# Kernel optimization log

Hardware: AMD Instinct MI355X
Metric: run time of the kernel (lower is better)

The kernel has to match this reference:

```python
import jax, jax.numpy as jnp
import numpy as np

N0 = N1 = 50000
E = 800000
IN = 128
OUT = 128
H = 8
DK = OUT // H  # 16
SQRT_DK = float(np.sqrt(DK))
T = 2  # node types


def setup_inputs() -> dict:
    key = jax.random.key(0)
    ks = jax.random.split(key, 24)
    s = 1.0 / np.sqrt(IN)
    inp = {
        "feat0": jax.random.normal(ks[0], (N0, IN), jnp.float32),
        "feat1": jax.random.normal(ks[1], (N1, IN), jnp.float32),
        "ev0": jax.random.uniform(ks[2], (E,), jnp.float32),
        "ev1": jax.random.uniform(ks[3], (E,), jnp.float32),
        "ev2": jax.random.uniform(ks[4], (E,), jnp.float32),
        "src0": jax.random.randint(ks[5], (E,), 0, N0),   # t0 -> t1
        "dst0": jax.random.randint(ks[6], (E,), 0, N1),
        "src1": jax.random.randint(ks[7], (E,), 0, N1),   # t1 -> t0
        "dst1": jax.random.randint(ks[8], (E,), 0, N0),
        "src2": jax.random.randint(ks[9], (E,), 0, N0),   # t0 -> t0
        "dst2": jax.random.randint(ks[10], (E,), 0, N0),
        # per-node-type parameters, stacked over T types
        "Kw": jax.random.normal(ks[11], (T, IN, OUT), jnp.float32) * s,
        "Kb": jnp.zeros((T, OUT), jnp.float32),
        "Qw": jax.random.normal(ks[12], (T, IN, OUT), jnp.float32) * s,
        "Qb": jnp.zeros((T, OUT), jnp.float32),
        "Vw": jax.random.normal(ks[13], (T, IN, OUT), jnp.float32) * s,
        "Vb": jnp.zeros((T, OUT), jnp.float32),
        "Aw": jax.random.normal(ks[14], (T, OUT, OUT), jnp.float32) * s,
        "Ab": jnp.zeros((T, OUT), jnp.float32),
        "ew": jax.random.normal(ks[15], (), jnp.float32),  # e_linear weight (1x1)
        "eb": jnp.zeros((), jnp.float32),                  # e_linear bias
        "skip": jnp.ones((T,), jnp.float32),
    }
    return inp


def _etype_agg(feat_s, feat_d, ts, td, src, dst, ev, n_dst,
               Kw, Kb, Qw, Qb, Vw, Vb, ew, eb):
    """One canonical etype: gather q.k per edge, edge_softmax over dst, u_mul_e + sum."""
    k = (feat_s @ Kw[ts] + Kb[ts]).reshape(-1, H, DK)
    v = (feat_s @ Vw[ts] + Vb[ts]).reshape(-1, H, DK)
    q = (feat_d @ Qw[td] + Qb[td]).reshape(-1, H, DK)
    # per-edge dot(q[dst], k[src]) over d_k -> [E, H]
    score = jnp.einsum('ehd,ehd->eh', q[dst], k[src])
    ea = ev[:, None] * ew + eb                     # e_linear on scalar edge feature, [E,1]
    score = score * ea / SQRT_DK                   # [E, H]
    # segmented softmax over incoming edges per destination node, per head
    m = jax.ops.segment_max(score, dst, num_segments=n_dst)
    ex = jnp.exp(score - m[dst])
    z = jax.ops.segment_sum(ex, dst, num_segments=n_dst)
    attn = ex / z[dst]                             # [E, H]
    msg = v[src] * attn[:, :, None]                # [E, H, DK]
    return jax.ops.segment_sum(msg, dst, num_segments=n_dst)  # [n_dst, H, DK]


def reference(feat0, feat1, ev0, ev1, ev2, src0, dst0, src1, dst1, src2, dst2,
              Kw, Kb, Qw, Qb, Vw, Vb, Aw, Ab, ew, eb, skip):
    # etype (t0,e0,t1)
    agg1 = _etype_agg(feat0, feat1, 0, 1, src0, dst0, ev0, N1,
                      Kw, Kb, Qw, Qb, Vw, Vb, ew, eb)
    # etypes targeting t0: (t1,e1,t0) and (t0,e2,t0); cross_reducer='mean'
    agg0a = _etype_agg(feat1, feat0, 1, 0, src1, dst1, ev1, N0,
                       Kw, Kb, Qw, Qb, Vw, Vb, ew, eb)
    agg0b = _etype_agg(feat0, feat0, 0, 0, src2, dst2, ev2, N0,
                       Kw, Kb, Qw, Qb, Vw, Vb, ew, eb)
    agg0 = 0.5 * (agg0a + agg0b)

    def _out(agg, feat, nid):
        t = agg.reshape(-1, OUT)
        trans = t @ Aw[nid] + Ab[nid]              # dropout omitted (eval mode)
        alpha = jax.nn.sigmoid(skip[nid])
        return trans * alpha + feat * (1.0 - alpha)

    h0 = _out(agg0, feat0, 0)
    h1 = _out(agg1, feat1, 1)
    return (h0, h1)
```

## Files before the change

### kernel.cpp

```cpp
#include <hip/hip_runtime.h>
#include <hip/hip_bf16.h>
#include <hip/hip_fp16.h>
#include <math.h>


#define NDIM 128
#define NRNG 32
#define NBK 512
#define UNITS (NBK * 4)
#define HSPAN 2048

typedef __attribute__((ext_vector_type(8))) short short8;
typedef __attribute__((ext_vector_type(4))) float f32x4;
typedef __attribute__((ext_vector_type(2))) _Float16 half2v;

__device__ __forceinline__ float bf2f(unsigned short u) {
    union { unsigned int i; float f; } x; x.i = ((unsigned int)u) << 16; return x.f;
}
__device__ __forceinline__ unsigned short f2bf(float f) {
    unsigned int u = __float_as_uint(f);
    unsigned int r = (u + 0x7FFFu + ((u >> 16) & 1u)) >> 16;
    return (unsigned short)r;
}
__device__ __forceinline__ int range_of(int d, int n) {
    return (int)(((long long)d * NRNG) / n);
}
union U4h { ushort4 u; struct { half2v a, b; } h; };

__global__ __launch_bounds__(256) void wt_prep(const float* __restrict__ Kw, const float* __restrict__ Qw,
                                               const float* __restrict__ Vw, const float* __restrict__ Aw,
                                               unsigned short* __restrict__ Wtbuf)
{
    const int b = blockIdx.x;
    const int t = b >> 2, m = b & 3;
    const float* src = (m == 0 ? Kw : m == 1 ? Qw : m == 2 ? Vw : Aw) + (size_t)t * 16384;
    unsigned short* dst = Wtbuf + (size_t)b * 16384;
    const int tid = threadIdx.x;
    __shared__ float tile[64][132];
#pragma unroll
    for (int h = 0; h < 2; ++h) {
        const int k0 = h * 64;
        for (int idx = tid; idx < 64 * 32; idx += 256) {
            const int kr = idx >> 5;
            const int c4 = (idx & 31) * 4;
            const float4 v = *(const float4*)(src + (size_t)(k0 + kr) * 128 + c4);
            tile[kr][c4 + 0] = v.x; tile[kr][c4 + 1] = v.y;
            tile[kr][c4 + 2] = v.z; tile[kr][c4 + 3] = v.w;
        }
        __syncthreads();
        for (int idx = tid; idx < 128 * 16; idx += 256) {
            const int nn = idx >> 4;
            const int kk4 = (idx & 15) * 4;
            ushort4 o;
            o.x = f2bf(tile[kk4 + 0][nn]); o.y = f2bf(tile[kk4 + 1][nn]);
            o.z = f2bf(tile[kk4 + 2][nn]); o.w = f2bf(tile[kk4 + 3][nn]);
            *(ushort4*)(dst + (size_t)nn * 128 + k0 + kk4) = o;
        }
        __syncthreads();
    }
}

__global__ __launch_bounds__(256) void gemm_kqv(
    const float* __restrict__ feat0, const float* __restrict__ feat1,
    const unsigned short* __restrict__ Wtbuf,
    const float* __restrict__ Kb, const float* __restrict__ Qb, const float* __restrict__ Vb,
    unsigned short* __restrict__ K0o, unsigned short* __restrict__ Q0o, unsigned short* __restrict__ V0o,
    unsigned short* __restrict__ K1o, unsigned short* __restrict__ Q1o, unsigned short* __restrict__ V1o,
    int n0, int n1, int blocks0)
{
    const int b = blockIdx.x;
    const bool t1 = (b >= blocks0);
    const float* feat = t1 ? feat1 : feat0;
    const int n = t1 ? n1 : n0;
    const int boff = t1 ? NDIM : 0;
    const unsigned short* Wt = Wtbuf + (t1 ? 4 * 16384 : 0);
    unsigned short* outs[3];
    outs[0] = t1 ? K1o : K0o; outs[1] = t1 ? Q1o : Q0o; outs[2] = t1 ? V1o : V0o;
    const float* biases[3] = {Kb + boff, Qb + boff, Vb + boff};

    const int tid = threadIdx.x;
    const int w = tid >> 6, lane = tid & 63;
    const int r16 = lane & 15, kg = lane >> 4;
    const int brow = (t1 ? b - blocks0 : b) * 64;
    const int arow = min(brow + w * 16 + r16, n - 1);

    __shared__ float sacc[64][129];

    short8 afr[4];
#pragma unroll
    for (int k0i = 0; k0i < 4; ++k0i) {
        const float* ap = feat + (size_t)arow * NDIM + k0i * 32 + kg * 8;
        const float4 lo = *(const float4*)ap;
        const float4 hi = *(const float4*)(ap + 4);
        short8 a;
        a[0] = (short)f2bf(lo.x); a[1] = (short)f2bf(lo.y);
        a[2] = (short)f2bf(lo.z); a[3] = (short)f2bf(lo.w);
        a[4] = (short)f2bf(hi.x); a[5] = (short)f2bf(hi.y);
        a[6] = (short)f2bf(hi.z); a[7] = (short)f2bf(hi.w);
        afr[k0i] = a;
    }
    const int c8 = (lane & 15) * 8;
#pragma unroll
    for (int m = 0; m < 3; ++m) {
        const unsigned short* wt = Wt + (size_t)m * 16384;
        f32x4 acc[8];
#pragma unroll
        for (int c = 0; c < 8; ++c) acc[c] = (f32x4){0.f, 0.f, 0.f, 0.f};
#pragma unroll
        for (int k0i = 0; k0i < 4; ++k0i)
#pragma unroll
            for (int c = 0; c < 8; ++c) {
                const short8 bb = *(const short8*)(wt + (size_t)(16 * c + r16) * NDIM + k0i * 32 + kg * 8);
                acc[c] = __builtin_amdgcn_mfma_f32_16x16x32_bf16(afr[k0i], bb, acc[c], 0, 0, 0);
            }
        __syncthreads();
#pragma unroll
        for (int c = 0; c < 8; ++c)
#pragma unroll
            for (int j = 0; j < 4; ++j)
                sacc[w * 16 + kg * 4 + j][16 * c + r16] = acc[c][j];
        __syncthreads();
        const float4 blo = *(const float4*)(biases[m] + c8);
        const float4 bhi = *(const float4*)(biases[m] + c8 + 4);
        const float bias8[8] = {blo.x, blo.y, blo.z, blo.w, bhi.x, bhi.y, bhi.z, bhi.w};
#pragma unroll
        for (int j = 0; j < 4; ++j) {
            const int rloc = w * 16 + (lane >> 4) + j * 4;
            const int grow = brow + rloc;
            if (grow < n) {
                short8 o;
#pragma unroll
                for (int i = 0; i < 8; ++i) {
                    const float x = sacc[rloc][c8 + i] + bias8[i];
                    o[i] = (m < 2) ? (short)__half_as_ushort(__float2half(x))
                                   : (short)f2bf(x);
                }
                *(short8*)(outs[m] + (size_t)grow * NDIM + c8) = o;
            }
        }
    }
}

__global__ __launch_bounds__(256) void gemm_out(
    const unsigned short* __restrict__ aggb0a, const unsigned short* __restrict__ aggb0b,
    const unsigned short* __restrict__ aggb1,
    const unsigned short* __restrict__ Wtbuf, const float* __restrict__ Ab,
    const float* __restrict__ feat0, const float* __restrict__ feat1,
    const float* __restrict__ skip, float* __restrict__ out,
    int n0, int n1, int blocks0)
{
    const int b = blockIdx.x;
    const bool t1 = (b >= blocks0);
    const int n = t1 ? n1 : n0;
    const unsigned short* A1 = t1 ? aggb1 : aggb0a;
    const unsigned short* A2 = t1 ? (const unsigned short*)nullptr : aggb0b;
    const unsigned short* Wt = Wtbuf + (t1 ? 7 : 3) * 16384;
    const float* bias = Ab + (t1 ? NDIM : 0);
    const float* feat = t1 ? feat1 : feat0;
    float* C = out + (t1 ? (size_t)n0 * NDIM : 0);
    const int nid = t1 ? 1 : 0;

    const int tid = threadIdx.x;
    const int w = tid >> 6, lane = tid & 63;
    const int r16 = lane & 15, kg = lane >> 4;
    const int brow = (t1 ? b - blocks0 : b) * 64;
    const int arow = min(brow + w * 16 + r16, n - 1);

    __shared__ float sacc[64][129];

    short8 afr[4];
#pragma unroll
    for (int k0i = 0; k0i < 4; ++k0i) {
        short8 a = *(const short8*)(A1 + (size_t)arow * NDIM + k0i * 32 + kg * 8);
        if (!t1) {
            const short8 bb = *(const short8*)(A2 + (size_t)arow * NDIM + k0i * 32 + kg * 8);
#pragma unroll
            for (int j = 0; j < 8; ++j) {
                const float v = 0.5f * (bf2f((unsigned short)a[j]) + bf2f((unsigned short)bb[j]));
                a[j] = (short)f2bf(v);
            }
        }
        afr[k0i] = a;
    }
    f32x4 acc[8];
#pragma unroll
    for (int c = 0; c < 8; ++c) acc[c] = (f32x4){0.f, 0.f, 0.f, 0.f};
#pragma unroll
    for (int k0i = 0; k0i < 4; ++k0i)
#pragma unroll
        for (int c = 0; c < 8; ++c) {
            const short8 bb = *(const short8*)(Wt + (size_t)(16 * c + r16) * NDIM + k0i * 32 + kg * 8);
            acc[c] = __builtin_amdgcn_mfma_f32_16x16x32_bf16(afr[k0i], bb, acc[c], 0, 0, 0);
        }
    __syncthreads();
#pragma unroll
    for (int c = 0; c < 8; ++c)
#pragma unroll
        for (int j = 0; j < 4; ++j)
            sacc[w * 16 + kg * 4 + j][16 * c + r16] = acc[c][j];
    __syncthreads();

    const float sk = skip[nid];
    const float alpha = 1.f / (1.f + __expf(-sk));
    const float beta = 1.f - alpha;
    const int c8 = (lane & 15) * 8;
    const float4 blo = *(const float4*)(bias + c8);
    const float4 bhi = *(const float4*)(bias + c8 + 4);
#pragma unroll
    for (int j = 0; j < 4; ++j) {
        const int rloc = w * 16 + (lane >> 4) + j * 4;
        const int grow = brow + rloc;
        if (grow < n) {
            const float4 fa = *(const float4*)(feat + (size_t)grow * NDIM + c8);
            const float4 fb = *(const float4*)(feat + (size_t)grow * NDIM + c8 + 4);
            float4 oa, ob;
            oa.x = (sacc[rloc][c8 + 0] + blo.x) * alpha + fa.x * beta;
            oa.y = (sacc[rloc][c8 + 1] + blo.y) * alpha + fa.y * beta;
            oa.z = (sacc[rloc][c8 + 2] + blo.z) * alpha + fa.z * beta;
            oa.w = (sacc[rloc][c8 + 3] + blo.w) * alpha + fa.w * beta;
            ob.x = (sacc[rloc][c8 + 4] + bhi.x) * alpha + fb.x * beta;
            ob.y = (sacc[rloc][c8 + 5] + bhi.y) * alpha + fb.y * beta;
            ob.z = (sacc[rloc][c8 + 6] + bhi.z) * alpha + fb.z * beta;
            ob.w = (sacc[rloc][c8 + 7] + bhi.w) * alpha + fb.w * beta;
            *(float4*)(C + (size_t)grow * NDIM + c8) = oa;
            *(float4*)(C + (size_t)grow * NDIM + c8 + 4) = ob;
        }
    }
}

__global__ __launch_bounds__(256) void bucket_count(
    const int* __restrict__ d0, int E0, const int* __restrict__ d1, int E1,
    const int* __restrict__ d2, int E2, int n0, int n1, int* __restrict__ cnts)
{
    const int seg = blockIdx.y;
    const int* dst = seg == 0 ? d0 : (seg == 1 ? d1 : d2);
    const int E = seg == 0 ? E0 : (seg == 1 ? E1 : E2);
    const int ns = seg == 0 ? n1 : n0;
    const int unit = blockIdx.x * 4 + (threadIdx.x >> 6);
    const int lane = threadIdx.x & 63;
    const int span = (E + UNITS - 1) / UNITS;
    const int b = unit * span;
    const int e = min(b + span, E);

    int run[NRNG];
#pragma unroll
    for (int r0 = 0; r0 < NRNG; ++r0) run[r0] = 0;
    for (int i0 = b; i0 < e; i0 += 64) {
        const int i = i0 + lane;
        const bool v = i < e;
        const int d = v ? dst[i] : 0;
        const unsigned int r = v ? (unsigned int)range_of(d, ns) : 0xFFu;
#pragma unroll
        for (int r0 = 0; r0 < NRNG; ++r0)
            run[r0] += __popcll(__ballot(r == (unsigned int)r0));
    }
    if (lane == 0) {
        int* c = cnts + ((size_t)seg * UNITS + unit) * NRNG;
#pragma unroll
        for (int r0 = 0; r0 < NRNG; ++r0) c[r0] = run[r0];
    }
}

__global__ __launch_bounds__(256) void bucket_scan(int* __restrict__ cnts, int* __restrict__ rcur)
{
    const int seg = blockIdx.x >> 5;
    const int r = blockIdx.x & 31;
    const int t = threadIdx.x, lane = t & 63, w = t >> 6;

    int v[8];
    int run = 0;
#pragma unroll
    for (int j = 0; j < 8; ++j) {
        const int u = t * 8 + j;
        const int x = cnts[((size_t)seg * UNITS + u) * NRNG + r];
        v[j] = run;
        run += x;
    }
    const int tsum = run;
    int x = tsum;
#pragma unroll
    for (int o = 1; o < 64; o <<= 1) {
        const int y = __shfl_up(x, o);
        if (lane >= o) x += y;
    }
    const int wexc = x - tsum;
    __shared__ int wsum[4];
    if (lane == 63) wsum[w] = x;
    __syncthreads();
    int wbase = 0;
    for (int i = 0; i < w; ++i) wbase += wsum[i];
    const int base = wbase + wexc;
#pragma unroll
    for (int j = 0; j < 8; ++j) {
        const int u = t * 8 + j;
        cnts[((size_t)seg * UNITS + u) * NRNG + r] = base + v[j];
    }
    if (t == 255) rcur[seg * NRNG + r] = base + tsum;
}

__global__ __launch_bounds__(256) void bucket_write(
    const int* __restrict__ d0, const int* __restrict__ s0, const float* __restrict__ e0, int E0,
    const int* __restrict__ d1, const int* __restrict__ s1, const float* __restrict__ e1, int E1,
    const int* __restrict__ d2, const int* __restrict__ s2, const float* __restrict__ e2, int E2,
    int n0, int n1, const float* __restrict__ ew, const float* __restrict__ eb,
    const int* __restrict__ cnts, uint2* __restrict__ stg, int cap)
{
    const int seg = blockIdx.y;
    const int* dst = seg == 0 ? d0 : (seg == 1 ? d1 : d2);
    const int* src = seg == 0 ? s0 : (seg == 1 ? s1 : s2);
    const float* ev = seg == 0 ? e0 : (seg == 1 ? e1 : e2);
    const int E = seg == 0 ? E0 : (seg == 1 ? E1 : E2);
    const int ns = seg == 0 ? n1 : n0;
    const int unit = blockIdx.x * 4 + (threadIdx.x >> 6);
    const int lane = threadIdx.x & 63;
    const int span = (E + UNITS - 1) / UNITS;
    const int b = unit * span;
    const int e = min(b + span, E);
    const float LOG2E = 1.4426950408889634f;
    const float ews = ew[0] * 0.25f * LOG2E;
    const float ebs = eb[0] * 0.25f * LOG2E;
    uint2* sbase = stg + (size_t)seg * NRNG * cap;

    int run[NRNG];
    {
        const int* c = cnts + ((size_t)seg * UNITS + unit) * NRNG;
#pragma unroll
        for (int r0 = 0; r0 < NRNG; ++r0) run[r0] = c[r0];
    }
    for (int i0 = b; i0 < e; i0 += 64) {
        const int i = i0 + lane;
        const bool v = i < e;
        int d = 0, s = 0; float ee = 0.f;
        if (v) { d = dst[i]; s = src[i]; ee = ev[i]; }
        const unsigned int r = v ? (unsigned int)range_of(d, ns) : 0xFFu;
#pragma unroll
        for (int r0 = 0; r0 < NRNG; ++r0) {
            const unsigned long long m = __ballot(r == (unsigned int)r0);
            if (m == 0ull) continue;
            if (r == (unsigned int)r0) {
                const int off = run[r0] + __popcll(m & ((1ull << lane) - 1ull));
                sbase[(size_t)r0 * cap + off] =
                    make_uint2((unsigned int)d | ((unsigned int)s << 16), __float_as_uint(ee * ews + ebs));
            }
            run[r0] += __popcll(m);
        }
    }
}

__global__ __launch_bounds__(1024) void sortB(
    const uint2* __restrict__ stg, int cap, const int* __restrict__ rcur,
    int nA, int* __restrict__ offA, unsigned int* __restrict__ gA,
    int nB, int* __restrict__ offB, unsigned int* __restrict__ gB,
    int nC, int* __restrict__ offC, unsigned int* __restrict__ gC)
{
    const int seg = blockIdx.y;
    const int r = blockIdx.x;
    const int n = seg == 0 ? nA : (seg == 1 ? nB : nC);
    int* off = seg == 0 ? offA : (seg == 1 ? offB : offC);
    unsigned int* edg = seg == 0 ? gA : (seg == 1 ? gB : gC);
    const int cnt = rcur[seg * NRNG + r];
    const uint2* s = stg + ((size_t)seg * NRNG + r) * cap;
    const int dbase = (int)(((long long)r * n + NRNG - 1) / NRNG);
    const int dnext = (int)(((long long)(r + 1) * n + NRNG - 1) / NRNG);
    const int span = dnext - dbase;
    int ebase = 0;
    for (int i = 0; i < r; ++i) ebase += rcur[seg * NRNG + i];

    __shared__ int hist[HSPAN];
    __shared__ int wsum[16];
    const int tid = threadIdx.x, lane = tid & 63, wid = tid >> 6;

    for (int i = tid; i < span; i += 1024) hist[i] = 0;
    __syncthreads();
    for (int i = tid; i < cnt; i += 1024)
        atomicAdd(&hist[(int)(s[i].x & 0xFFFFu) - dbase], 1);
    __syncthreads();
    const int C = (span + 1023) >> 10;
    int v[4];
    int run = 0;
    const int b0 = tid * C;
#pragma unroll 4
    for (int j = 0; j < C; ++j) {
        const int i = b0 + j;
        const int x = (i < span) ? hist[i] : 0;
        v[j] = run;
        run += x;
    }
    int x = run;
#pragma unroll
    for (int o = 1; o < 64; o <<= 1) {
        const int y = __shfl_up(x, o);
        if (lane >= o) x += y;
    }
    if (lane == 63) wsum[wid] = x;
    __syncthreads();
    int wbase = 0;
    for (int i = 0; i < wid; ++i) wbase += wsum[i];
    const int tb = ebase + wbase + (x - run);
#pragma unroll 4
    for (int j = 0; j < C; ++j) {
        const int i = b0 + j;
        if (i < span) hist[i] = tb + v[j];
    }
    __syncthreads();
    for (int i = tid; i < span; i += 1024) off[dbase + i] = hist[i];
    if (r == NRNG - 1 && tid == 0) off[n] = ebase + cnt;
    __syncthreads();
    for (int i = tid; i < cnt; i += 1024) {
        const uint2 e = s[i];
        const int d = (int)(e.x & 0xFFFFu);
        const int p = atomicAdd(&hist[d - dbase], 1);
        const float wf = __uint_as_float(e.y);
        const __half hh = __float2half(wf);
        edg[p] = (e.x >> 16) | ((unsigned int)__half_as_ushort(hh) << 16);
    }
}

__global__ __launch_bounds__(256) void edge_agg3(
    const int* __restrict__ off0, const unsigned int* __restrict__ edg0,
    const unsigned short* __restrict__ K0e, const unsigned short* __restrict__ Q0e,
    const unsigned short* __restrict__ V0e, unsigned short* __restrict__ out0, int nd0,
    const int* __restrict__ off1, const unsigned int* __restrict__ edg1,
    const unsigned short* __restrict__ K1e, const unsigned short* __restrict__ Q1e,
    const unsigned short* __restrict__ V1e, unsigned short* __restrict__ out1, int nd1,
    const int* __restrict__ off2, const unsigned int* __restrict__ edg2,
    const unsigned short* __restrict__ K2e, const unsigned short* __restrict__ Q2e,
    const unsigned short* __restrict__ V2e, unsigned short* __restrict__ out2, int nd2)
{
    const int seg = blockIdx.y;
    const int* off = seg == 0 ? off0 : (seg == 1 ? off1 : off2);
    const unsigned int* edg = seg == 0 ? edg0 : (seg == 1 ? edg1 : edg2);
    const unsigned short* K = seg == 0 ? K0e : (seg == 1 ? K1e : K2e);
    const unsigned short* Q = seg == 0 ? Q0e : (seg == 1 ? Q1e : Q2e);
    const unsigned short* V = seg == 0 ? V0e : (seg == 1 ? V1e : V2e);
    unsigned short* aggb = seg == 0 ? out0 : (seg == 1 ? out1 : out2);
    const int n_dst = seg == 0 ? nd0 : (seg == 1 ? nd1 : nd2);

    const int wv = (blockIdx.x * blockDim.x + threadIdx.x) >> 6;
    const int lane = threadIdx.x & 63;
    const int half = lane >> 5, l5 = lane & 31;
    const int dst = 2 * wv + half;
    const bool valid = dst < n_dst;
    int beg = 0, len = 0;
    if (valid) { beg = off[dst]; len = off[dst + 1] - beg; }
    const int maxLen = max(len, __shfl_xor(len, 32));
    if (maxLen == 0) {
        if (valid) *(ushort4*)(aggb + (size_t)dst * NDIM + 4 * l5) = (ushort4){0, 0, 0, 0};
        return;
    }
    U4h q;
    q.u = make_ushort4(0, 0, 0, 0);
    if (valid) q.u = *(const ushort4*)(Q + (size_t)dst * NDIM + 4 * l5);
    const half2v q01 = q.h.a, q23 = q.h.b;

    float zA = 0.f, aA0 = 0.f, aA1 = 0.f, aA2 = 0.f, aA3 = 0.f;
    float zB = 0.f, aB0 = 0.f, aB1 = 0.f, aB2 = 0.f, aB3 = 0.f;

    unsigned int ec = (l5 < len) ? edg[beg + l5] : 0u;
    for (int t0 = 0; t0 < maxLen; t0 += 32) {
        unsigned int en = 0u;
        const int t0n = t0 + 32;
        if (t0n < maxLen && t0n + l5 < len) en = edg[beg + t0n + l5];
        const int lim = min(32, maxLen - t0);
        for (int u = 0; u < lim; u += 2) {
            const int sl0 = (half << 5) + u;
            const unsigned int v0 = (unsigned int)__shfl((int)ec, sl0);
            const unsigned int v1 = (unsigned int)__shfl((int)ec, sl0 + 1);
            const bool act0 = (t0 + u) < len;
            const bool act1 = (u + 1 < lim) && ((t0 + u + 1) < len);
            const int s0 = (int)(v0 & 0xFFFFu);
            const int s1 = (int)(v1 & 0xFFFFu);
            const float w0 = __half2float(__ushort_as_half((unsigned short)(v0 >> 16)));
            const float w1 = __half2float(__ushort_as_half((unsigned short)(v1 >> 16)));
            U4h k0u, k1u;
            k0u.u = *(const ushort4*)(K + (size_t)s0 * NDIM + 4 * l5);
            k1u.u = *(const ushort4*)(K + (size_t)s1 * NDIM + 4 * l5);
            const ushort4 vr0 = *(const ushort4*)(V + (size_t)s0 * NDIM + 4 * l5);
            const ushort4 vr1 = *(const ushort4*)(V + (size_t)s1 * NDIM + 4 * l5);
#if __has_builtin(__builtin_amdgcn_fdot2)
            float d0 = __builtin_amdgcn_fdot2(k0u.h.a, q01, 0.f, false);
            d0 = __builtin_amdgcn_fdot2(k0u.h.b, q23, d0, false);
            float d1 = __builtin_amdgcn_fdot2(k1u.h.a, q01, 0.f, false);
            d1 = __builtin_amdgcn_fdot2(k1u.h.b, q23, d1, false);
#else
            float d0 = (float)k0u.h.a[0] * (float)q01[0] + (float)k0u.h.a[1] * (float)q01[1]
                     + (float)k0u.h.b[0] * (float)q23[0] + (float)k0u.h.b[1] * (float)q23[1];
            float d1 = (float)k1u.h.a[0] * (float)q01[0] + (float)k1u.h.a[1] * (float)q01[1]
                     + (float)k1u.h.b[0] * (float)q23[0] + (float)k1u.h.b[1] * (float)q23[1];
#endif
            d0 += __shfl_xor(d0, 1);
            d1 += __shfl_xor(d1, 1);
            d0 += __shfl_xor(d0, 2);
            d1 += __shfl_xor(d1, 2);
            const float p0 = act0 ? exp2f(d0 * w0) : 0.f;
            const float p1 = act1 ? exp2f(d1 * w1) : 0.f;
            zA += p0;
            aA0 += p0 * bf2f(vr0.x); aA1 += p0 * bf2f(vr0.y);
            aA2 += p0 * bf2f(vr0.z); aA3 += p0 * bf2f(vr0.w);
            zB += p1;
            aB0 += p1 * bf2f(vr1.x); aB1 += p1 * bf2f(vr1.y);
            aB2 += p1 * bf2f(vr1.z); aB3 += p1 * bf2f(vr1.w);
        }
        ec = en;
    }
    if (valid) {
        const float z = zA + zB;
        const float inv = (len > 0) ? 1.f / z : 0.f;
        ushort4 o;
        o.x = f2bf((aA0 + aB0) * inv); o.y = f2bf((aA1 + aB1) * inv);
        o.z = f2bf((aA2 + aB2) * inv); o.w = f2bf((aA3 + aB3) * inv);
        *(ushort4*)(aggb + (size_t)dst * NDIM + 4 * l5) = o;
    }
}

extern "C" void kernel_launch(void* const* d_in, const int* in_sizes, int n_in,
                              void* d_out, int out_size, void* d_ws, size_t ws_size,
                              hipStream_t stream)
{
    const float* feat0 = (const float*)d_in[0];
    const float* feat1 = (const float*)d_in[1];
    const float* ev0 = (const float*)d_in[2];
    const float* ev1 = (const float*)d_in[3];
    const float* ev2 = (const float*)d_in[4];
    const int* src0 = (const int*)d_in[5];
    const int* dst0 = (const int*)d_in[6];
    const int* src1 = (const int*)d_in[7];
    const int* dst1 = (const int*)d_in[8];
    const int* src2 = (const int*)d_in[9];
    const int* dst2 = (const int*)d_in[10];
    const float* Kw = (const float*)d_in[11];
    const float* Kb = (const float*)d_in[12];
    const float* Qw = (const float*)d_in[13];
    const float* Qb = (const float*)d_in[14];
    const float* Vw = (const float*)d_in[15];
    const float* Vb = (const float*)d_in[16];
    const float* Aw = (const float*)d_in[17];
    const float* Ab = (const float*)d_in[18];
    const float* ew = (const float*)d_in[19];
    const float* eb = (const float*)d_in[20];
    const float* skip = (const float*)d_in[21];

    const int n0 = in_sizes[0] / NDIM;
    const int n1 = in_sizes[1] / NDIM;
    const int E0 = in_sizes[5];
    const int E1 = in_sizes[7];
    const int E2 = in_sizes[9];
    if (max(n0, n1) > 65504) return;
    const int Emax = max(E0, max(E1, E2));
    const int cap = Emax / NRNG + 8192;

    auto rup = [](size_t b) { return (b + 255) & ~size_t(255); };
    const size_t need =
        rup((size_t)8 * 16384 * 2) +
        rup((size_t)n0 * NDIM * 2) * 3 +
        rup((size_t)n1 * NDIM * 2) * 3 +
        rup((size_t)n1 * NDIM * 2) +
        rup((size_t)n0 * NDIM * 2) * 2 +
        rup((size_t)(n1 + 1) * 4) +
        rup((size_t)(n0 + 1) * 4) * 2 +
        rup((size_t)128 * 4) +
        rup((size_t)3 * UNITS * NRNG * 4) +
        rup((size_t)3 * NRNG * cap * 8) +
        rup((size_t)E0 * 4) + rup((size_t)E1 * 4) + rup((size_t)E2 * 4);
    if (ws_size < need) return;

    char* p = (char*)d_ws;
    auto alloc = [&](size_t bytes) -> char* {
        char* r = p;
        p += (bytes + 255) & ~size_t(255);
        return r;
    };
    unsigned short* Wtbuf = (unsigned short*)alloc((size_t)8 * 16384 * 2);
    unsigned short* K0 = (unsigned short*)alloc((size_t)n0 * NDIM * 2);
    unsigned short* Q0 = (unsigned short*)alloc((size_t)n0 * NDIM * 2);
    unsigned short* V0 = (unsigned short*)alloc((size_t)n0 * NDIM * 2);
    unsigned short* K1 = (unsigned short*)alloc((size_t)n1 * NDIM * 2);
    unsigned short* Q1 = (unsigned short*)alloc((size_t)n1 * NDIM * 2);
    unsigned short* V1 = (unsigned short*)alloc((size_t)n1 * NDIM * 2);
    unsigned short* aggb1  = (unsigned short*)alloc((size_t)n1 * NDIM * 2);
    unsigned short* aggb0a = (unsigned short*)alloc((size_t)n0 * NDIM * 2);
    unsigned short* aggb0b = (unsigned short*)alloc((size_t)n0 * NDIM * 2);
    int* off0 = (int*)alloc((size_t)(n1 + 1) * 4);
    int* off1 = (int*)alloc((size_t)(n0 + 1) * 4);
    int* off2 = (int*)alloc((size_t)(n0 + 1) * 4);
    int* rcur = (int*)alloc((size_t)128 * 4);
    int* cnts = (int*)alloc((size_t)3 * UNITS * NRNG * 4);
    uint2* stg = (uint2*)alloc((size_t)3 * NRNG * cap * 8);
    unsigned int* edg0 = (unsigned int*)alloc((size_t)E0 * 4);
    unsigned int* edg1 = (unsigned int*)alloc((size_t)E1 * 4);
    unsigned int* edg2 = (unsigned int*)alloc((size_t)E2 * 4);

    dim3 blk(256);
    const int blocks0 = (n0 + 63) / 64, blocks1 = (n1 + 63) / 64;

    wt_prep<<<8, 256, 0, stream>>>(Kw, Qw, Vw, Aw, Wtbuf);
    gemm_kqv<<<blocks0 + blocks1, blk, 0, stream>>>(feat0, feat1, Wtbuf, Kb, Qb, Vb,
                                                    K0, Q0, V0, K1, Q1, V1, n0, n1, blocks0);

    bucket_count<<<dim3(NBK, 3), blk, 0, stream>>>(dst0, E0, dst1, E1, dst2, E2, n0, n1, cnts);
    bucket_scan<<<3 * NRNG, blk, 0, stream>>>(cnts, rcur);
    bucket_write<<<dim3(NBK, 3), blk, 0, stream>>>(dst0, src0, ev0, E0,
                                                   dst1, src1, ev1, E1,
                                                   dst2, src2, ev2, E2,
                                                   n0, n1, ew, eb, cnts, stg, cap);
    sortB<<<dim3(NRNG, 3), 1024, 0, stream>>>(stg, cap, rcur,
                                              n1, off0, edg0,
                                              n0, off1, edg1,
                                              n0, off2, edg2);

    const int nmax = (n0 > n1) ? n0 : n1;
    const int ebx = ((nmax + 1) / 2 + 3) / 4;
    edge_agg3<<<dim3(ebx, 3), blk, 0, stream>>>(
        off0, edg0, K0, Q1, V0, aggb1, n1,
        off1, edg1, K1, Q0, V1, aggb0a, n0,
        off2, edg2, K0, Q0, V0, aggb0b, n0);

    gemm_out<<<blocks0 + blocks1, blk, 0, stream>>>(aggb0a, aggb0b, aggb1, Wtbuf, Ab,
                                                    feat0, feat1, skip, (float*)d_out,
                                                    n0, n1, blocks0);
}
```

Baseline: 396.0 us.

## Merge weight prep with bucket count and K/Q/V GEMM with bucket write

Weight transposition now runs inside the bucket-count kernel, and the K/Q/V projection GEMM runs inside the bucket-write kernel, with GEMM and write blocks interleaved by block index. This cuts two kernel launches and lets independent compute-bound GEMM work overlap with memory-bound edge bucketing on the GPU. The cost is higher register and LDS pressure, since the shared sacc buffer is allocated even for write blocks, which could lower occupancy for the bucketing role.

```diff
diff --git a/kernel.cpp b/kernel.cpp
--- a/kernel.cpp
+++ b/kernel.cpp
@@ -27,217 +27,51 @@
 }
 union U4h { ushort4 u; struct { half2v a, b; } h; };
 
-__global__ __launch_bounds__(256) void wt_prep(const float* __restrict__ Kw, const float* __restrict__ Qw,
-                                               const float* __restrict__ Vw, const float* __restrict__ Aw,
-                                               unsigned short* __restrict__ Wtbuf)
-{
-    const int b = blockIdx.x;
-    const int t = b >> 2, m = b & 3;
-    const float* src = (m == 0 ? Kw : m == 1 ? Qw : m == 2 ? Vw : Aw) + (size_t)t * 16384;
-    unsigned short* dst = Wtbuf + (size_t)b * 16384;
-    const int tid = threadIdx.x;
-    __shared__ float tile[64][132];
-#pragma unroll
-    for (int h = 0; h < 2; ++h) {
-        const int k0 = h * 64;
-        for (int idx = tid; idx < 64 * 32; idx += 256) {
-            const int kr = idx >> 5;
-            const int c4 = (idx & 31) * 4;
-            const float4 v = *(const float4*)(src + (size_t)(k0 + kr) * 128 + c4);
-            tile[kr][c4 + 0] = v.x; tile[kr][c4 + 1] = v.y;
-            tile[kr][c4 + 2] = v.z; tile[kr][c4 + 3] = v.w;
-        }
-        __syncthreads();
-        for (int idx = tid; idx < 128 * 16; idx += 256) {
-            const int nn = idx >> 4;
-            const int kk4 = (idx & 15) * 4;
-            ushort4 o;
-            o.x = f2bf(tile[kk4 + 0][nn]); o.y = f2bf(tile[kk4 + 1][nn]);
-            o.z = f2bf(tile[kk4 + 2][nn]); o.w = f2bf(tile[kk4 + 3][nn]);
-            *(ushort4*)(dst + (size_t)nn * 128 + k0 + kk4) = o;
-        }
-        __syncthreads();
-    }
-}
-
-__global__ __launch_bounds__(256) void gemm_kqv(
-    const float* __restrict__ feat0, const float* __restrict__ feat1,
-    const unsigned short* __restrict__ Wtbuf,
-    const float* __restrict__ Kb, const float* __restrict__ Qb, const float* __restrict__ Vb,
-    unsigned short* __restrict__ K0o, unsigned short* __restrict__ Q0o, unsigned short* __restrict__ V0o,
-    unsigned short* __restrict__ K1o, unsigned short* __restrict__ Q1o, unsigned short* __restrict__ V1o,
-    int n0, int n1, int blocks0)
-{
-    const int b = blockIdx.x;
-    const bool t1 = (b >= blocks0);
-    const float* feat = t1 ? feat1 : feat0;
-    const int n = t1 ? n1 : n0;
-    const int boff = t1 ? NDIM : 0;
-    const unsigned short* Wt = Wtbuf + (t1 ? 4 * 16384 : 0);
-    unsigned short* outs[3];
-    outs[0] = t1 ? K1o : K0o; outs[1] = t1 ? Q1o : Q0o; outs[2] = t1 ? V1o : V0o;
-    const float* biases[3] = {Kb + boff, Qb + boff, Vb + boff};
-
-    const int tid = threadIdx.x;
-    const int w = tid >> 6, lane = tid & 63;
-    const int r16 = lane & 15, kg = lane >> 4;
-    const int brow = (t1 ? b - blocks0 : b) * 64;
-    const int arow = min(brow + w * 16 + r16, n - 1);
-
-    __shared__ float sacc[64][129];
-
-    short8 afr[4];
-#pragma unroll
-    for (int k0i = 0; k0i < 4; ++k0i) {
-        const float* ap = feat + (size_t)arow * NDIM + k0i * 32 + kg * 8;
-        const float4 lo = *(const float4*)ap;
-        const float4 hi = *(const float4*)(ap + 4);
-        short8 a;
-        a[0] = (short)f2bf(lo.x); a[1] = (short)f2bf(lo.y);
-        a[2] = (short)f2bf(lo.z); a[3] = (short)f2bf(lo.w);
-        a[4] = (short)f2bf(hi.x); a[5] = (short)f2bf(hi.y);
-        a[6] = (short)f2bf(hi.z); a[7] = (short)f2bf(hi.w);
-        afr[k0i] = a;
-    }
-    const int c8 = (lane & 15) * 8;
-#pragma unroll
-    for (int m = 0; m < 3; ++m) {
-        const unsigned short* wt = Wt + (size_t)m * 16384;
-        f32x4 acc[8];
-#pragma unroll
-        for (int c = 0; c < 8; ++c) acc[c] = (f32x4){0.f, 0.f, 0.f, 0.f};
-#pragma unroll
-        for (int k0i = 0; k0i < 4; ++k0i)
-#pragma unroll
-            for (int c = 0; c < 8; ++c) {
-                const short8 bb = *(const short8*)(wt + (size_t)(16 * c + r16) * NDIM + k0i * 32 + kg * 8);
-                acc[c] = __builtin_amdgcn_mfma_f32_16x16x32_bf16(afr[k0i], bb, acc[c], 0, 0, 0);
-            }
-        __syncthreads();
-#pragma unroll
-        for (int c = 0; c < 8; ++c)
-#pragma unroll
-            for (int j = 0; j < 4; ++j)
-                sacc[w * 16 + kg * 4 + j][16 * c + r16] = acc[c][j];
-        __syncthreads();
-        const float4 blo = *(const float4*)(biases[m] + c8);
-        const float4 bhi = *(const float4*)(biases[m] + c8 + 4);
-        const float bias8[8] = {blo.x, blo.y, blo.z, blo.w, bhi.x, bhi.y, bhi.z, bhi.w};
-#pragma unroll
-        for (int j = 0; j < 4; ++j) {
-            const int rloc = w * 16 + (lane >> 4) + j * 4;
-            const int grow = brow + rloc;
-            if (grow < n) {
-                short8 o;
-#pragma unroll
-                for (int i = 0; i < 8; ++i) {
-                    const float x = sacc[rloc][c8 + i] + bias8[i];
-                    o[i] = (m < 2) ? (short)__half_as_ushort(__float2half(x))
-                                   : (short)f2bf(x);
-                }
-                *(short8*)(outs[m] + (size_t)grow * NDIM + c8) = o;
-            }
-        }
-    }
-}
-
-__global__ __launch_bounds__(256) void gemm_out(
-    const unsigned short* __restrict__ aggb0a, const unsigned short* __restrict__ aggb0b,
-    const unsigned short* __restrict__ aggb1,
-    const unsigned short* __restrict__ Wtbuf, const float* __restrict__ Ab,
-    const float* __restrict__ feat0, const float* __restrict__ feat1,
-    const float* __restrict__ skip, float* __restrict__ out,
-    int n0, int n1, int blocks0)
-{
-    const int b = blockIdx.x;
-    const bool t1 = (b >= blocks0);
-    const int n = t1 ? n1 : n0;
-    const unsigned short* A1 = t1 ? aggb1 : aggb0a;
-    const unsigned short* A2 = t1 ? (const unsigned short*)nullptr : aggb0b;
-    const unsigned short* Wt = Wtbuf + (t1 ? 7 : 3) * 16384;
-    const float* bias = Ab + (t1 ? NDIM : 0);
-    const float* feat = t1 ? feat1 : feat0;
-    float* C = out + (t1 ? (size_t)n0 * NDIM : 0);
-    const int nid = t1 ? 1 : 0;
-
-    const int tid = threadIdx.x;
-    const int w = tid >> 6, lane = tid & 63;
-    const int r16 = lane & 15, kg = lane >> 4;
-    const int brow = (t1 ? b - blocks0 : b) * 64;
-    const int arow = min(brow + w * 16 + r16, n - 1);
-
-    __shared__ float sacc[64][129];
-
-    short8 afr[4];
-#pragma unroll
-    for (int k0i = 0; k0i < 4; ++k0i) {
-        short8 a = *(const short8*)(A1 + (size_t)arow * NDIM + k0i * 32 + kg * 8);
-        if (!t1) {
-            const short8 bb = *(const short8*)(A2 + (size_t)arow * NDIM + k0i * 32 + kg * 8);
-#pragma unroll
-            for (int j = 0; j < 8; ++j) {
-                const float v = 0.5f * (bf2f((unsigned short)a[j]) + bf2f((unsigned short)bb[j]));
-                a[j] = (short)f2bf(v);
-            }
-        }
-        afr[k0i] = a;
-    }
-    f32x4 acc[8];
-#pragma unroll
-    for (int c = 0; c < 8; ++c) acc[c] = (f32x4){0.f, 0.f, 0.f, 0.f};
-#pragma unroll
-    for (int k0i = 0; k0i < 4; ++k0i)
-#pragma unroll
-        for (int c = 0; c < 8; ++c) {
-            const short8 bb = *(const short8*)(Wt + (size_t)(16 * c + r16) * NDIM + k0i * 32 + kg * 8);
-            acc[c] = __builtin_amdgcn_mfma_f32_16x16x32_bf16(afr[k0i], bb, acc[c], 0, 0, 0);
-        }
-    __syncthreads();
-#pragma unroll
-    for (int c = 0; c < 8; ++c)
-#pragma unroll
-        for (int j = 0; j < 4; ++j)
-            sacc[w * 16 + kg * 4 + j][16 * c + r16] = acc[c][j];
-    __syncthreads();
-
-    const float sk = skip[nid];
-    const float alpha = 1.f / (1.f + __expf(-sk));
-    const float beta = 1.f - alpha;
-    const int c8 = (lane & 15) * 8;
-    const float4 blo = *(const float4*)(bias + c8);
-    const float4 bhi = *(const float4*)(bias + c8 + 4);
-#pragma unroll
-    for (int j = 0; j < 4; ++j) {
-        const int rloc = w * 16 + (lane >> 4) + j * 4;
-        const int grow = brow + rloc;
-        if (grow < n) {
-            const float4 fa = *(const float4*)(feat + (size_t)grow * NDIM + c8);
-            const float4 fb = *(const float4*)(feat + (size_t)grow * NDIM + c8 + 4);
-            float4 oa, ob;
-            oa.x = (sacc[rloc][c8 + 0] + blo.x) * alpha + fa.x * beta;
-            oa.y = (sacc[rloc][c8 + 1] + blo.y) * alpha + fa.y * beta;
-            oa.z = (sacc[rloc][c8 + 2] + blo.z) * alpha + fa.z * beta;
-            oa.w = (sacc[rloc][c8 + 3] + blo.w) * alpha + fa.w * beta;
-            ob.x = (sacc[rloc][c8 + 4] + bhi.x) * alpha + fb.x * beta;
-            ob.y = (sacc[rloc][c8 + 5] + bhi.y) * alpha + fb.y * beta;
-            ob.z = (sacc[rloc][c8 + 6] + bhi.z) * alpha + fb.z * beta;
-            ob.w = (sacc[rloc][c8 + 7] + bhi.w) * alpha + fb.w * beta;
-            *(float4*)(C + (size_t)grow * NDIM + c8) = oa;
-            *(float4*)(C + (size_t)grow * NDIM + c8 + 4) = ob;
-        }
-    }
-}
-
-__global__ __launch_bounds__(256) void bucket_count(
+__global__ __launch_bounds__(256) void prep_count(
+    const float* __restrict__ Kw, const float* __restrict__ Qw,
+    const float* __restrict__ Vw, const float* __restrict__ Aw,
+    unsigned short* __restrict__ Wtbuf,
     const int* __restrict__ d0, int E0, const int* __restrict__ d1, int E1,
     const int* __restrict__ d2, int E2, int n0, int n1, int* __restrict__ cnts)
 {
-    const int seg = blockIdx.y;
+    __shared__ float tile[64][132];
+    const int tid = threadIdx.x;
+    if (blockIdx.x < 8) {
+        const int b = blockIdx.x;
+        const int t = b >> 2, m = b & 3;
+        const float* src = (m == 0 ? Kw : m == 1 ? Qw : m == 2 ? Vw : Aw) + (size_t)t * 16384;
+        unsigned short* dst = Wtbuf + (size_t)b * 16384;
+#pragma unroll
+        for (int h = 0; h < 2; ++h) {
+            const int k0 = h * 64;
+            for (int idx = tid; idx < 64 * 32; idx += 256) {
+                const int kr = idx >> 5;
+                const int c4 = (idx & 31) * 4;
+                const float4 v = *(const float4*)(src + (size_t)(k0 + kr) * 128 + c4);
+                tile[kr][c4 + 0] = v.x; tile[kr][c4 + 1] = v.y;
+                tile[kr][c4 + 2] = v.z; tile[kr][c4 + 3] = v.w;
+            }
+            __syncthreads();
+            for (int idx = tid; idx < 128 * 16; idx += 256) {
+                const int nn = idx >> 4;
+                const int kk4 = (idx & 15) * 4;
+                ushort4 o;
+                o.x = f2bf(tile[kk4 + 0][nn]); o.y = f2bf(tile[kk4 + 1][nn]);
+                o.z = f2bf(tile[kk4 + 2][nn]); o.w = f2bf(tile[kk4 + 3][nn]);
+                *(ushort4*)(dst + (size_t)nn * 128 + k0 + kk4) = o;
+            }
+            __syncthreads();
+        }
+        return;
+    }
+    const int idx0 = blockIdx.x - 8;
+    const int seg = idx0 / NBK;
+    const int bx = idx0 - seg * NBK;
     const int* dst = seg == 0 ? d0 : (seg == 1 ? d1 : d2);
     const int E = seg == 0 ? E0 : (seg == 1 ? E1 : E2);
     const int ns = seg == 0 ? n1 : n0;
-    const int unit = blockIdx.x * 4 + (threadIdx.x >> 6);
-    const int lane = threadIdx.x & 63;
+    const int unit = bx * 4 + (tid >> 6);
+    const int lane = tid & 63;
     const int span = (E + UNITS - 1) / UNITS;
     const int b = unit * span;
     const int e = min(b + span, E);
@@ -298,21 +132,114 @@
     if (t == 255) rcur[seg * NRNG + r] = base + tsum;
 }
 
-__global__ __launch_bounds__(256) void bucket_write(
-    const int* __restrict__ d0, const int* __restrict__ s0, const float* __restrict__ e0, int E0,
-    const int* __restrict__ d1, const int* __restrict__ s1, const float* __restrict__ e1, int E1,
-    const int* __restrict__ d2, const int* __restrict__ s2, const float* __restrict__ e2, int E2,
-    int n0, int n1, const float* __restrict__ ew, const float* __restrict__ eb,
+__global__ __launch_bounds__(256) void gemm_write(
+    const float* __restrict__ feat0, const float* __restrict__ feat1,
+    const unsigned short* __restrict__ Wtbuf,
+    const float* __restrict__ Kb, const float* __restrict__ Qb, const float* __restrict__ Vb,
+    unsigned short* __restrict__ K0o, unsigned short* __restrict__ Q0o, unsigned short* __restrict__ V0o,
+    unsigned short* __restrict__ K1o, unsigned short* __restrict__ Q1o, unsigned short* __restrict__ V1o,
+    int n0, int n1, int blocks0, int Gblocks,
+    const int* __restrict__ wd0, const int* __restrict__ ws0, const float* __restrict__ we0, int E0,
+    const int* __restrict__ wd1, const int* __restrict__ ws1, const float* __restrict__ we1, int E1,
+    const int* __restrict__ wd2, const int* __restrict__ ws2, const float* __restrict__ we2, int E2,
+    const float* __restrict__ ew, const float* __restrict__ eb,
     const int* __restrict__ cnts, uint2* __restrict__ stg, int cap)
 {
-    const int seg = blockIdx.y;
-    const int* dst = seg == 0 ? d0 : (seg == 1 ? d1 : d2);
-    const int* src = seg == 0 ? s0 : (seg == 1 ? s1 : s2);
-    const float* ev = seg == 0 ? e0 : (seg == 1 ? e1 : e2);
+    const int W = 3 * NBK;
+    const int G = Gblocks;
+    const int mn2 = 2 * min(G, W);
+    int role, sub;
+    {
+        const int idx = blockIdx.x;
+        if (idx < mn2) { role = idx & 1; sub = idx >> 1; }
+        else {
+            const int rem = idx - mn2;
+            if (G > W) { role = 0; sub = min(G, W) + rem; }
+            else       { role = 1; sub = min(G, W) + rem; }
+        }
+    }
+    const int tid = threadIdx.x;
+    __shared__ float sacc[64][129];
+
+    if (role == 0) {
+        const bool t1 = (sub >= blocks0);
+        const float* feat = t1 ? feat1 : feat0;
+        const int n = t1 ? n1 : n0;
+        const int boff = t1 ? NDIM : 0;
+        const unsigned short* Wt = Wtbuf + (t1 ? 4 * 16384 : 0);
+        unsigned short* outs[3];
+        outs[0] = t1 ? K1o : K0o; outs[1] = t1 ? Q1o : Q0o; outs[2] = t1 ? V1o : V0o;
+        const float* biases[3] = {Kb + boff, Qb + boff, Vb + boff};
+
+        const int w = tid >> 6, lane = tid & 63;
+        const int r16 = lane & 15, kg = lane >> 4;
+        const int brow = (t1 ? sub - blocks0 : sub) * 64;
+        const int arow = min(brow + w * 16 + r16, n - 1);
+
+        short8 afr[4];
+#pragma unroll
+        for (int k0i = 0; k0i < 4; ++k0i) {
+            const float* ap = feat + (size_t)arow * NDIM + k0i * 32 + kg * 8;
+            const float4 lo = *(const float4*)ap;
+            const float4 hi = *(const float4*)(ap + 4);
+            short8 a;
+            a[0] = (short)f2bf(lo.x); a[1] = (short)f2bf(lo.y);
+            a[2] = (short)f2bf(lo.z); a[3] = (short)f2bf(lo.w);
+            a[4] = (short)f2bf(hi.x); a[5] = (short)f2bf(hi.y);
+            a[6] = (short)f2bf(hi.z); a[7] = (short)f2bf(hi.w);
+            afr[k0i] = a;
+        }
+        const int c8 = (lane & 15) * 8;
+#pragma unroll
+        for (int m = 0; m < 3; ++m) {
+            const unsigned short* wt = Wt + (size_t)m * 16384;
+            f32x4 acc[8];
+#pragma unroll
+            for (int c = 0; c < 8; ++c) acc[c] = (f32x4){0.f, 0.f, 0.f, 0.f};
+#pragma unroll
+            for (int k0i = 0; k0i < 4; ++k0i)
+#pragma unroll
+                for (int c = 0; c < 8; ++c) {
+                    const short8 bb = *(const short8*)(wt + (size_t)(16 * c + r16) * NDIM + k0i * 32 + kg * 8);
+                    acc[c] = __builtin_amdgcn_mfma_f32_16x16x32_bf16(afr[k0i], bb, acc[c], 0, 0, 0);
+                }
+            __syncthreads();
+#pragma unroll
+            for (int c = 0; c < 8; ++c)
+#pragma unroll
+                for (int j = 0; j < 4; ++j)
+                    sacc[w * 16 + kg * 4 + j][16 * c + r16] = acc[c][j];
+            __syncthreads();
+            const float4 blo = *(const float4*)(biases[m] + c8);
+            const float4 bhi = *(const float4*)(biases[m] + c8 + 4);
+            const float bias8[8] = {blo.x, blo.y, blo.z, blo.w, bhi.x, bhi.y, bhi.z, bhi.w};
+#pragma unroll
+            for (int j = 0; j < 4; ++j) {
+                const int rloc = w * 16 + (lane >> 4) + j * 4;
+                const int grow = brow + rloc;
+                if (grow < n) {
+                    short8 o;
+#pragma unroll
+                    for (int i = 0; i < 8; ++i) {
+                        const float x = sacc[rloc][c8 + i] + bias8[i];
+                        o[i] = (m < 2) ? (short)__half_as_ushort(__float2half(x))
+                                       : (short)f2bf(x);
+                    }
+                    *(short8*)(outs[m] + (size_t)grow * NDIM + c8) = o;
+                }
+            }
+        }
+        return;
+    }
+    const int seg = sub / NBK;
+    const int bx = sub - seg * NBK;
+    const int* dst = seg == 0 ? wd0 : (seg == 1 ? wd1 : wd2);
+    const int* src = seg == 0 ? ws0 : (seg == 1 ? ws1 : ws2);
+    const float* ev = seg == 0 ? we0 : (seg == 1 ? we1 : we2);
     const int E = seg == 0 ? E0 : (seg == 1 ? E1 : E2);
     const int ns = seg == 0 ? n1 : n0;
-    const int unit = blockIdx.x * 4 + (threadIdx.x >> 6);
-    const int lane = threadIdx.x & 63;
+    const int unit = bx * 4 + (tid >> 6);
+    const int lane = tid & 63;
     const int span = (E + UNITS - 1) / UNITS;
     const int b = unit * span;
     const int e = min(b + span, E);
@@ -513,6 +440,93 @@
     }
 }
 
+__global__ __launch_bounds__(256) void gemm_out(
+    const unsigned short* __restrict__ aggb0a, const unsigned short* __restrict__ aggb0b,
+    const unsigned short* __restrict__ aggb1,
+    const unsigned short* __restrict__ Wtbuf, const float* __restrict__ Ab,
+    const float* __restrict__ feat0, const float* __restrict__ feat1,
+    const float* __restrict__ skip, float* __restrict__ out,
+    int n0, int n1, int blocks0)
+{
+    const int b = blockIdx.x;
+    const bool t1 = (b >= blocks0);
+    const int n = t1 ? n1 : n0;
+    const unsigned short* A1 = t1 ? aggb1 : aggb0a;
+    const unsigned short* A2 = t1 ? (const unsigned short*)nullptr : aggb0b;
+    const unsigned short* Wt = Wtbuf + (t1 ? 7 : 3) * 16384;
+    const float* bias = Ab + (t1 ? NDIM : 0);
+    const float* feat = t1 ? feat1 : feat0;
+    float* C = out + (t1 ? (size_t)n0 * NDIM : 0);
+    const int nid = t1 ? 1 : 0;
+
+    const int tid = threadIdx.x;
+    const int w = tid >> 6, lane = tid & 63;
+    const int r16 = lane & 15, kg = lane >> 4;
+    const int brow = (t1 ? b - blocks0 : b) * 64;
+    const int arow = min(brow + w * 16 + r16, n - 1);
+
+    __shared__ float sacc[64][129];
+
+    short8 afr[4];
+#pragma unroll
+    for (int k0i = 0; k0i < 4; ++k0i) {
+        short8 a = *(const short8*)(A1 + (size_t)arow * NDIM + k0i * 32 + kg * 8);
+        if (!t1) {
+            const short8 bb = *(const short8*)(A2 + (size_t)arow * NDIM + k0i * 32 + kg * 8);
+#pragma unroll
+            for (int j = 0; j < 8; ++j) {
+                const float v = 0.5f * (bf2f((unsigned short)a[j]) + bf2f((unsigned short)bb[j]));
+                a[j] = (short)f2bf(v);
+            }
+        }
+        afr[k0i] = a;
+    }
+    f32x4 acc[8];
+#pragma unroll
+    for (int c = 0; c < 8; ++c) acc[c] = (f32x4){0.f, 0.f, 0.f, 0.f};
+#pragma unroll
+    for (int k0i = 0; k0i < 4; ++k0i)
+#pragma unroll
+        for (int c = 0; c < 8; ++c) {
+            const short8 bb = *(const short8*)(Wt + (size_t)(16 * c + r16) * NDIM + k0i * 32 + kg * 8);
+            acc[c] = __builtin_amdgcn_mfma_f32_16x16x32_bf16(afr[k0i], bb, acc[c], 0, 0, 0);
+        }
+    __syncthreads();
+#pragma unroll
+    for (int c = 0; c < 8; ++c)
+#pragma unroll
+        for (int j = 0; j < 4; ++j)
+            sacc[w * 16 + kg * 4 + j][16 * c + r16] = acc[c][j];
+    __syncthreads();
+
+    const float sk = skip[nid];
+    const float alpha = 1.f / (1.f + __expf(-sk));
+    const float beta = 1.f - alpha;
+    const int c8 = (lane & 15) * 8;
+    const float4 blo = *(const float4*)(bias + c8);
+    const float4 bhi = *(const float4*)(bias + c8 + 4);
+#pragma unroll
+    for (int j = 0; j < 4; ++j) {
+        const int rloc = w * 16 + (lane >> 4) + j * 4;
+        const int grow = brow + rloc;
+        if (grow < n) {
+            const float4 fa = *(const float4*)(feat + (size_t)grow * NDIM + c8);
+            const float4 fb = *(const float4*)(feat + (size_t)grow * NDIM + c8 + 4);
+            float4 oa, ob;
+            oa.x = (sacc[rloc][c8 + 0] + blo.x) * alpha + fa.x * beta;
+            oa.y = (sacc[rloc][c8 + 1] + blo.y) * alpha + fa.y * beta;
+            oa.z = (sacc[rloc][c8 + 2] + blo.z) * alpha + fa.z * beta;
+            oa.w = (sacc[rloc][c8 + 3] + blo.w) * alpha + fa.w * beta;
+            ob.x = (sacc[rloc][c8 + 4] + bhi.x) * alpha + fb.x * beta;
+            ob.y = (sacc[rloc][c8 + 5] + bhi.y) * alpha + fb.y * beta;
+            ob.z = (sacc[rloc][c8 + 6] + bhi.z) * alpha + fb.z * beta;
+            ob.w = (sacc[rloc][c8 + 7] + bhi.w) * alpha + fb.w * beta;
+            *(float4*)(C + (size_t)grow * NDIM + c8) = oa;
+            *(float4*)(C + (size_t)grow * NDIM + c8 + 4) = ob;
+        }
+    }
+}
+
 extern "C" void kernel_launch(void* const* d_in, const int* in_sizes, int n_in,
                               void* d_out, int out_size, void* d_ws, size_t ws_size,
                               hipStream_t stream)
@@ -592,17 +606,17 @@
 
     dim3 blk(256);
     const int blocks0 = (n0 + 63) / 64, blocks1 = (n1 + 63) / 64;
-
-    wt_prep<<<8, 256, 0, stream>>>(Kw, Qw, Vw, Aw, Wtbuf);
-    gemm_kqv<<<blocks0 + blocks1, blk, 0, stream>>>(feat0, feat1, Wtbuf, Kb, Qb, Vb,
-                                                    K0, Q0, V0, K1, Q1, V1, n0, n1, blocks0);
-
-    bucket_count<<<dim3(NBK, 3), blk, 0, stream>>>(dst0, E0, dst1, E1, dst2, E2, n0, n1, cnts);
+    const int G = blocks0 + blocks1;
+
+    prep_count<<<8 + 3 * NBK, blk, 0, stream>>>(Kw, Qw, Vw, Aw, Wtbuf,
+                                                dst0, E0, dst1, E1, dst2, E2, n0, n1, cnts);
     bucket_scan<<<3 * NRNG, blk, 0, stream>>>(cnts, rcur);
-    bucket_write<<<dim3(NBK, 3), blk, 0, stream>>>(dst0, src0, ev0, E0,
-                                                   dst1, src1, ev1, E1,
-                                                   dst2, src2, ev2, E2,
-                                                   n0, n1, ew, eb, cnts, stg, cap);
+    gemm_write<<<G + 3 * NBK, blk, 0, stream>>>(feat0, feat1, Wtbuf, Kb, Qb, Vb,
+                                                K0, Q0, V0, K1, Q1, V1, n0, n1, blocks0, G,
+                                                dst0, src0, ev0, E0,
+                                                dst1, src1, ev1, E1,
+                                                dst2, src2, ev2, E2,
+                                                ew, eb, cnts, stg, cap);
     sortB<<<dim3(NRNG, 3), 1024, 0, stream>>>(stg, cap, rcur,
                                               n1, off0, edg0,
                                               n0, off1, edg1,
@@ -615,7 +629,7 @@
         off1, edg1, K1, Q0, V1, aggb0a, n0,
         off2, edg2, K0, Q0, V0, aggb0b, n0);
 
-    gemm_out<<<blocks0 + blocks1, blk, 0, stream>>>(aggb0a, aggb0b, aggb1, Wtbuf, Ab,
-                                                    feat0, feat1, skip, (float*)d_out,
-                                                    n0, n1, blocks0);
-}
+    gemm_out<<<G, blk, 0, stream>>>(aggb0a, aggb0b, aggb1, Wtbuf, Ab,
+                                    feat0, feat1, skip, (float*)d_out,
+                                    n0, n1, blocks0);
+}
```

After: 420.4 us. +6.2%, slower.
